# Performance work log

Measured on AMD Instinct MI355X. Metric: run time of the kernel, lower is better.

## Reference

```python
import jax, jax.numpy as jnp
import numpy as np

NEG_SLOPE = 0.2  # PyG GATConv default


def gat_layer(x, src, dst, W, att_src, att_dst, bias, num_nodes):
    """One PyG-style GATConv (concat=True, add_self_loops handled by caller).
    x: [N, F_in], W: [F_in, H*C], att_src/att_dst: [H, C], bias: [H*C].
    """
    H, C = att_src.shape
    h = (x @ W).reshape(num_nodes, H, C)              # [N, H, C]
    a_src = (h * att_src).sum(-1)                     # [N, H]
    a_dst = (h * att_dst).sum(-1)                     # [N, H]
    e = jax.nn.leaky_relu(a_src[src] + a_dst[dst], NEG_SLOPE)  # [E, H]
    # segment softmax over destination neighborhoods
    m = jax.ops.segment_max(e, dst, num_segments=num_nodes)   # [N, H]
    ex = jnp.exp(e - m[dst])
    denom = jax.ops.segment_sum(ex, dst, num_segments=num_nodes)
    alpha = ex / denom[dst]                           # [E, H]
    out = jax.ops.segment_sum(alpha[:, :, None] * h[src], dst,
                              num_segments=num_nodes)  # [N, H, C]
    return out.reshape(num_nodes, H * C) + bias


def setup_inputs() -> dict:
    key = jax.random.key(0)
    ks = jax.random.split(key, 12)
    N, E, D, H = 50000, 800000, 128, 8
    C = D // H
    x = jax.random.normal(ks[0], (N, D), dtype=jnp.float32)
    edge_index = jax.random.randint(ks[1], (2, E), 0, N, dtype=jnp.int64)
    s = 0.1
    return {
        "x": x,
        "edge_index": edge_index,
        "W1": s * jax.random.normal(ks[2], (D, H * C), dtype=jnp.float32),
        "as1": s * jax.random.normal(ks[3], (H, C), dtype=jnp.float32),
        "ad1": s * jax.random.normal(ks[4], (H, C), dtype=jnp.float32),
        "b1": jnp.zeros((H * C,), dtype=jnp.float32),
        "W2": s * jax.random.normal(ks[5], (D, H * C), dtype=jnp.float32),
        "as2": s * jax.random.normal(ks[6], (H, C), dtype=jnp.float32),
        "ad2": s * jax.random.normal(ks[7], (H, C), dtype=jnp.float32),
        "b2": jnp.zeros((H * C,), dtype=jnp.float32),
    }


def reference(x, edge_index, W1, as1, ad1, b1, W2, as2, ad2, b2):
    n = x.shape[0]
    # PyG GATConv default add_self_loops=True
    loop = jnp.arange(n, dtype=edge_index.dtype)
    src = jnp.concatenate([edge_index[0], loop])
    dst = jnp.concatenate([edge_index[1], loop])
    h = jax.nn.relu(gat_layer(x, src, dst, W1, as1, ad1, b1, n))
    # dropout p=0.5 is identity in eval mode
    return gat_layer(h, src, dst, W2, as2, ad2, b2, n)
```

## Files before the change

### kernel.cpp

```cpp
#include <hip/hip_runtime.h>
#include <math.h>

#define D 128
#define H 8
#define C 16
#define NEG_SLOPE 0.2f
#define SCAN_TILE 1024

typedef unsigned short ushortT;
typedef __attribute__((ext_vector_type(8))) short short8;
typedef __attribute__((ext_vector_type(4))) float f32x4;

__device__ __forceinline__ float bf2f(unsigned short v) {
    union { unsigned int i; float f; } c;
    c.i = ((unsigned int)v) << 16;
    return c.f;
}
__device__ __forceinline__ unsigned short f2bf(float f) {
    union { float f; unsigned int i; } c;
    c.f = f;
    unsigned int lsb = (c.i >> 16) & 1u;
    c.i += 0x7fffu + lsb;
    return (unsigned short)(c.i >> 16);
}



__global__ void k_hist(const int* __restrict__ ei, int* cursor,
                       int* __restrict__ rank, int E, int n) {
    int i4 = (blockIdx.x * blockDim.x + threadIdx.x) * 4;
    if (((E & 3) == 0) && i4 + 3 < E) {
        int4 dv = *(const int4*)(ei + (size_t)E + i4);
        int4 r;
        r.x = atomicAdd(cursor + dv.x, 1);
        r.y = atomicAdd(cursor + dv.y, 1);
        r.z = atomicAdd(cursor + dv.z, 1);
        r.w = atomicAdd(cursor + dv.w, 1);
        *(int4*)(rank + i4) = r;
    } else {
        for (int k = i4; k < E && k < i4 + 4; k++)
            rank[k] = atomicAdd(cursor + ei[(size_t)E + k], 1);
    }
}

__device__ __forceinline__ int padc(int c) { return (c + 4) & ~3; }

__global__ __launch_bounds__(256) void k_scan_partial(
    const int* __restrict__ cursor, int* __restrict__ bsum, int n) {
    __shared__ int lds[256];
    int t = threadIdx.x;
    int base = blockIdx.x * SCAN_TILE + t * 4;
    int s = 0;
    if (base + 3 < n) {
        int4 v = *(const int4*)(cursor + base);
        s = padc(v.x) + padc(v.y) + padc(v.z) + padc(v.w);
    } else {
        for (int k = 0; k < 4; k++)
            if (base + k < n) s += padc(cursor[base + k]);
    }
    lds[t] = s;
    __syncthreads();
    for (int st = 128; st > 0; st >>= 1) {
        if (t < st) lds[t] += lds[t + st];
        __syncthreads();
    }
    if (t == 0) bsum[blockIdx.x] = lds[0];
}

__global__ void k_scan_bsum(int* bsum, int nb) {
    if (threadIdx.x == 0 && blockIdx.x == 0) {
        int run = 0;
        for (int i = 0; i < nb; i++) {
            int v = bsum[i];
            bsum[i] = run;
            run += v;
        }
    }
}

__global__ __launch_bounds__(256) void k_scan_final(
    const int* __restrict__ cursor, int* __restrict__ poffs,
    const int* __restrict__ bsum, int* __restrict__ csrsrc, int n) {
    __shared__ int lds[256];
    int t = threadIdx.x;
    int base = blockIdx.x * SCAN_TILE + t * 4;
    int c[4] = {0, 0, 0, 0};
    if (base + 3 < n) {
        int4 q = *(const int4*)(cursor + base);
        c[0] = q.x; c[1] = q.y; c[2] = q.z; c[3] = q.w;
    } else {
        for (int k = 0; k < 4; k++)
            if (base + k < n) c[k] = cursor[base + k];
    }
    int s = padc(c[0]) + padc(c[1]) + padc(c[2]) + padc(c[3]);
    lds[t] = s;
    __syncthreads();
    for (int st = 1; st < 256; st <<= 1) {
        int add = (t >= st) ? lds[t - st] : 0;
        __syncthreads();
        lds[t] += add;
        __syncthreads();
    }
    int run = bsum[blockIdx.x] + ((t == 0) ? 0 : lds[t - 1]);
    if (blockIdx.x == 0 && t == 0) poffs[0] = 0;
#pragma unroll
    for (int k = 0; k < 4; k++) {
        int i = base + k;
        if (i < n) {
            int pv = padc(c[k]);
            csrsrc[run + c[k]] = i;
            for (int k2 = c[k] + 1; k2 < pv; k2++)
                csrsrc[run + k2] = n;
            run += pv;
            poffs[i + 1] = run;
        }
    }
}

__global__ void k_fill(const int* __restrict__ ei, const int* __restrict__ poffs,
                       const int* __restrict__ rank, int* __restrict__ csrsrc,
                       ushortT* __restrict__ hbuf, float* __restrict__ asrc,
                       int E, int n) {
    int tid = blockIdx.x * blockDim.x + threadIdx.x;
    int E4 = (E + 3) >> 2;
    if (tid < E4) {
        int i4 = tid * 4;
        if (((E & 3) == 0) && i4 + 3 < E) {
            int4 sv = *(const int4*)(ei + i4);
            int4 dv = *(const int4*)(ei + (size_t)E + i4);
            int4 rv = *(const int4*)(rank + i4);
            csrsrc[poffs[dv.x] + rv.x] = sv.x;
            csrsrc[poffs[dv.y] + rv.y] = sv.y;
            csrsrc[poffs[dv.z] + rv.z] = sv.z;
            csrsrc[poffs[dv.w] + rv.w] = sv.w;
        } else {
            for (int k = i4; k < E && k < i4 + 4; k++)
                csrsrc[poffs[ei[(size_t)E + k]] + rank[k]] = ei[k];
        }
    } else if (tid == E4) {
        int total = poffs[n];
        for (int k = 0; k < 8; k++) csrsrc[total + k] = n;
        for (int k = 0; k < D; k++) hbuf[(size_t)n * D + k] = 0;
        for (int h = 0; h < H; h++) asrc[n * H + h] = -1e30f;
    }
}


__global__ __launch_bounds__(256) void k_xsplit(
    const float* __restrict__ x, ushortT* __restrict__ xh,
    ushortT* __restrict__ xl, int n, int nt16) {
    int idx = blockIdx.x * 256 + threadIdx.x;
    int r = idx >> 4;
    if (r >= nt16 * 16) return;
    int kb = idx & 15;
    float4 v0 = make_float4(0.f, 0.f, 0.f, 0.f), v1 = v0;
    if (r < n) {
        v0 = ((const float4*)(x + (size_t)r * D + kb * 8))[0];
        v1 = ((const float4*)(x + (size_t)r * D + kb * 8))[1];
    }
    int wt = r >> 4, m = r & 15, kt = kb >> 2, quad = kb & 3;
    int base = ((wt * 4 + kt) * 64 + (m + 16 * quad)) * 8;
    ushort4 h0, l0, h1, l1;
    h0.x = f2bf(v0.x); l0.x = f2bf(v0.x - bf2f(h0.x));
    h0.y = f2bf(v0.y); l0.y = f2bf(v0.y - bf2f(h0.y));
    h0.z = f2bf(v0.z); l0.z = f2bf(v0.z - bf2f(h0.z));
    h0.w = f2bf(v0.w); l0.w = f2bf(v0.w - bf2f(h0.w));
    h1.x = f2bf(v1.x); l1.x = f2bf(v1.x - bf2f(h1.x));
    h1.y = f2bf(v1.y); l1.y = f2bf(v1.y - bf2f(h1.y));
    h1.z = f2bf(v1.z); l1.z = f2bf(v1.z - bf2f(h1.z));
    h1.w = f2bf(v1.w); l1.w = f2bf(v1.w - bf2f(h1.w));
    *(ushort4*)(xh + base) = h0;
    *(ushort4*)(xh + base + 4) = h1;
    *(ushort4*)(xl + base) = l0;
    *(ushort4*)(xl + base + 4) = l1;
}


__global__ __launch_bounds__(256) void k_wprep(
    const float* __restrict__ W1, const float* __restrict__ as1,
    const float* __restrict__ ad1, const float* __restrict__ W2,
    const float* __restrict__ as2, const float* __restrict__ ad2,
    ushortT* __restrict__ wf1_hi, ushortT* __restrict__ wf1_lo,
    ushortT* __restrict__ wf2_hi, ushortT* __restrict__ wf2_lo) {
    int b = blockIdx.x;
    const float *W, *att_s, *att_d;
    ushortT *whi, *wlo;
    int idx;
    if (b < 9) {
        W = W1; att_s = as1; att_d = ad1; whi = wf1_hi; wlo = wf1_lo;
        idx = b * 256 + threadIdx.x;
    } else {
        W = W2; att_s = as2; att_d = ad2; whi = wf2_hi; wlo = wf2_lo;
        idx = (b - 9) * 256 + threadIdx.x;
    }
    if (idx >= 4 * 9 * 64) return;
    int lane = idx & 63;
    int nt = (idx >> 6) % 9;
    int kt = idx / (9 * 64);
    int quad = lane >> 4, ncol = lane & 15;
#pragma unroll
    for (int j = 0; j < 8; j++) {
        int k = kt * 32 + quad * 8 + j;
        float v;
        if (nt < 8) {
            v = W[k * D + nt * 16 + ncol];
        } else {
            const float* att = (ncol < 8) ? att_s : att_d;
            int hd = ncol & 7;
            float s = 0.f;
            for (int c = 0; c < 16; c++)
                s += W[k * D + hd * 16 + c] * att[hd * 16 + c];
            v = s;
        }
        unsigned short hi = f2bf(v);
        unsigned short lo = f2bf(v - bf2f(hi));
        whi[idx * 8 + j] = hi;
        wlo[idx * 8 + j] = lo;
    }
}


__global__ __launch_bounds__(256) void k_gemm_att(
    const ushortT* __restrict__ xh, const ushortT* __restrict__ xl,
    const ushortT* __restrict__ wf_hi, const ushortT* __restrict__ wf_lo,
    ushortT* __restrict__ hout, float* __restrict__ as_,
    float* __restrict__ ad_, int n) {
    int t = threadIdx.x;
    int wt = blockIdx.x * 4 + (t >> 6);
    if (wt * 16 >= n) return;
    int lane = t & 63;

    f32x4 acc[9];
#pragma unroll
    for (int nt = 0; nt < 9; nt++) acc[nt] = (f32x4){0.f, 0.f, 0.f, 0.f};

#pragma unroll
    for (int kt = 0; kt < 4; kt++) {
        const ushortT* ax = xh + (size_t)((wt * 4 + kt) * 64 + lane) * 8;
        short8 a_hi = *(const short8*)ax;
        short8 a_lo = *(const short8*)(xl + (size_t)((wt * 4 + kt) * 64 + lane) * 8);
        const ushortT* bh = wf_hi + (size_t)(kt * 576 + lane) * 8;
        const ushortT* bl = wf_lo + (size_t)(kt * 576 + lane) * 8;
#pragma unroll
        for (int nt = 0; nt < 9; nt++) {
            short8 b_hi = *(const short8*)(bh + nt * 512);
            short8 b_lo = *(const short8*)(bl + nt * 512);
            acc[nt] = __builtin_amdgcn_mfma_f32_16x16x32_bf16(a_hi, b_hi, acc[nt], 0, 0, 0);
            acc[nt] = __builtin_amdgcn_mfma_f32_16x16x32_bf16(a_lo, b_hi, acc[nt], 0, 0, 0);
            acc[nt] = __builtin_amdgcn_mfma_f32_16x16x32_bf16(a_hi, b_lo, acc[nt], 0, 0, 0);
        }
    }

    int q = lane >> 4, ncol = lane & 15;
    int rbase = wt * 16 + q * 4;
#pragma unroll
    for (int nt = 0; nt < 8; nt++) {
#pragma unroll
        for (int reg = 0; reg < 4; reg++) {
            int r = rbase + reg;
            if (r < n) hout[(size_t)r * D + nt * 16 + ncol] = f2bf(acc[nt][reg]);
        }
    }
#pragma unroll
    for (int reg = 0; reg < 4; reg++) {
        int r = rbase + reg;
        if (r < n) {
            float v = acc[8][reg];
            if (ncol < 8) as_[r * H + ncol] = v;
            else          ad_[r * H + (ncol - 8)] = v;
        }
    }
}


__global__ __launch_bounds__(256) void k_aggregate(
    const ushortT* __restrict__ hbuf, const float* __restrict__ asrc,
    const float* __restrict__ adst, const int* __restrict__ csr,
    const int* __restrict__ poffs, const float* __restrict__ bias,
    float* __restrict__ out, ushortT* __restrict__ oh, ushortT* __restrict__ ol,
    int out_mode, int n) {
    int t = threadIdx.x;
    int d = blockIdx.x * 8 + (t >> 5);
    if (d >= n) return;
    int ll = t & 31;
    int h = ll >> 2;

    int off = poffs[d];
    int degp = poffs[d + 1] - off;
    float adh = adst[d * H + h];

    float4 acc0 = make_float4(0.f, 0.f, 0.f, 0.f);
    float4 acc1 = make_float4(0.f, 0.f, 0.f, 0.f);
    float ssum = 0.f;

    int s0 = csr[off + 0], s1 = csr[off + 1], s2 = csr[off + 2], s3 = csr[off + 3];
    for (int j = 0; j < degp; j += 4) {
        int p0 = csr[off + j + 4], p1 = csr[off + j + 5];
        int p2 = csr[off + j + 6], p3 = csr[off + j + 7];
        float e0 = asrc[s0 * H + h] + adh;
        float e1 = asrc[s1 * H + h] + adh;
        float e2 = asrc[s2 * H + h] + adh;
        float e3 = asrc[s3 * H + h] + adh;
        ushort4 u0 = *(const ushort4*)(hbuf + (size_t)s0 * D + ll * 4);
        ushort4 u1 = *(const ushort4*)(hbuf + (size_t)s1 * D + ll * 4);
        ushort4 u2 = *(const ushort4*)(hbuf + (size_t)s2 * D + ll * 4);
        ushort4 u3 = *(const ushort4*)(hbuf + (size_t)s3 * D + ll * 4);
        float w0 = __expf(e0 > 0.f ? e0 : NEG_SLOPE * e0);
        float w1 = __expf(e1 > 0.f ? e1 : NEG_SLOPE * e1);
        float w2 = __expf(e2 > 0.f ? e2 : NEG_SLOPE * e2);
        float w3 = __expf(e3 > 0.f ? e3 : NEG_SLOPE * e3);
        ssum += (w0 + w1) + (w2 + w3);
        acc0.x += w0 * bf2f(u0.x); acc0.y += w0 * bf2f(u0.y);
        acc0.z += w0 * bf2f(u0.z); acc0.w += w0 * bf2f(u0.w);
        acc1.x += w1 * bf2f(u1.x); acc1.y += w1 * bf2f(u1.y);
        acc1.z += w1 * bf2f(u1.z); acc1.w += w1 * bf2f(u1.w);
        acc0.x += w2 * bf2f(u2.x); acc0.y += w2 * bf2f(u2.y);
        acc0.z += w2 * bf2f(u2.z); acc0.w += w2 * bf2f(u2.w);
        acc1.x += w3 * bf2f(u3.x); acc1.y += w3 * bf2f(u3.y);
        acc1.z += w3 * bf2f(u3.z); acc1.w += w3 * bf2f(u3.w);
        s0 = p0; s1 = p1; s2 = p2; s3 = p3;
    }

    float inv = 1.f / ssum;
    float4 b = ((const float4*)bias)[ll];
    float4 r;
    r.x = (acc0.x + acc1.x) * inv + b.x;
    r.y = (acc0.y + acc1.y) * inv + b.y;
    r.z = (acc0.z + acc1.z) * inv + b.z;
    r.w = (acc0.w + acc1.w) * inv + b.w;

    if (out_mode == 0) {
        ((float4*)(out + (size_t)d * D))[ll] = r;
    } else {
        r.x = fmaxf(r.x, 0.f);
        r.y = fmaxf(r.y, 0.f);
        r.z = fmaxf(r.z, 0.f);
        r.w = fmaxf(r.w, 0.f);
        int wt = d >> 4, m = d & 15;
        int kt = ll >> 3, quad = (ll >> 1) & 3, j0 = (ll & 1) * 4;
        int base = ((wt * 4 + kt) * 64 + (m + 16 * quad)) * 8 + j0;
        ushort4 hv, lv;
        hv.x = f2bf(r.x); lv.x = f2bf(r.x - bf2f(hv.x));
        hv.y = f2bf(r.y); lv.y = f2bf(r.y - bf2f(hv.y));
        hv.z = f2bf(r.z); lv.z = f2bf(r.z - bf2f(hv.z));
        hv.w = f2bf(r.w); lv.w = f2bf(r.w - bf2f(hv.w));
        *(ushort4*)(oh + base) = hv;
        *(ushort4*)(ol + base) = lv;
    }
}


extern "C" void kernel_launch(void* const* d_in, const int* in_sizes, int n_in,
                              void* d_out, int out_size, void* d_ws, size_t ws_size,
                              hipStream_t stream) {
    const float* x   = (const float*)d_in[0];
    const int*   ei  = (const int*)d_in[1];
    const float* W1  = (const float*)d_in[2];
    const float* as1 = (const float*)d_in[3];
    const float* ad1 = (const float*)d_in[4];
    const float* b1  = (const float*)d_in[5];
    const float* W2  = (const float*)d_in[6];
    const float* as2 = (const float*)d_in[7];
    const float* ad2 = (const float*)d_in[8];
    const float* b2  = (const float*)d_in[9];
    float* out = (float*)d_out;

    int N = in_sizes[0] / D;
    int E = in_sizes[1] / 2;
    int NT16 = (N + 15) / 16;
    int nb_scan = (N + SCAN_TILE - 1) / SCAN_TILE;
    const int WFN = 4 * 9 * 64 * 8;
    size_t XS = (size_t)NT16 * 2048;

    ushortT* hbuf = (ushortT*)d_ws;
    ushortT* xsh  = hbuf + (size_t)(N + 1) * D;
    ushortT* xsl  = xsh + XS;
    float* asrc = (float*)(xsl + XS);
    float* adst = asrc + (size_t)(N + 1) * H;
    int*   poffs  = (int*)(adst + (size_t)N * H);
    int*   cursor = poffs + ((N + 1 + 3) & ~3);
    int*   bsum   = cursor + ((N + 3) & ~3);
    int*   rank   = bsum + ((nb_scan + 3) & ~3);
    int*   csrsrc = rank + ((E + 3) & ~3);
    ushortT* wf1_hi = (ushortT*)(csrsrc + ((E + 4 * N + 8 + 3) & ~3));
    ushortT* wf1_lo = wf1_hi + WFN;
    ushortT* wf2_hi = wf1_lo + WFN;
    ushortT* wf2_lo = wf2_hi + WFN;

    hipMemsetAsync(cursor, 0, (size_t)N * sizeof(int), stream);

    int nb;
    nb = ((E + 3) / 4 + 255) / 256;
    k_hist<<<nb, 256, 0, stream>>>(ei, cursor, rank, E, N);
    k_scan_partial<<<nb_scan, 256, 0, stream>>>(cursor, bsum, N);
    k_scan_bsum<<<1, 64, 0, stream>>>(bsum, nb_scan);
    k_scan_final<<<nb_scan, 256, 0, stream>>>(cursor, poffs, bsum, csrsrc, N);
    nb = ((E + 3) / 4 + 1 + 255) / 256;
    k_fill<<<nb, 256, 0, stream>>>(ei, poffs, rank, csrsrc, hbuf, asrc, E, N);

    k_wprep<<<18, 256, 0, stream>>>(W1, as1, ad1, W2, as2, ad2,
                                    wf1_hi, wf1_lo, wf2_hi, wf2_lo);
    k_xsplit<<<NT16, 256, 0, stream>>>(x, xsh, xsl, N, NT16);

    int gb = (NT16 + 3) / 4;
    int ab = (N + 7) / 8;
    k_gemm_att<<<gb, 256, 0, stream>>>(xsh, xsl, wf1_hi, wf1_lo, hbuf, asrc, adst, N);
    k_aggregate<<<ab, 256, 0, stream>>>(hbuf, asrc, adst, csrsrc, poffs, b1,
                                        out, xsh, xsl, 1, N);
    k_gemm_att<<<gb, 256, 0, stream>>>(xsh, xsl, wf2_hi, wf2_lo, hbuf, asrc, adst, N);
    k_aggregate<<<ab, 256, 0, stream>>>(hbuf, asrc, adst, csrsrc, poffs, b2,
                                        out, xsh, xsl, 0, N);
}
```

Before: 277.7 us.

## Merge preprocessing kernels and use single-pass decoupled-lookback scan

Merges histogram, weight prep and x split into one launch, and replaces the three-kernel scan with a single kernel that spins on per-block published sums. It also fuses the CSR fill with the first GEMM into one grid of disjoint block ranges. The aim is to cut launch count and serialization gaps between small kernels. The lookback relies on all earlier scan blocks being resident, and sstate is sized to 64 blocks. That fits N=50000 (49 blocks) but would hang or overflow for larger graphs.

```diff
diff --git a/kernel.cpp b/kernel.cpp
--- a/kernel.cpp
+++ b/kernel.cpp
@@ -24,11 +24,14 @@
     return (unsigned short)(c.i >> 16);
 }
 
-
-
-__global__ void k_hist(const int* __restrict__ ei, int* cursor,
-                       int* __restrict__ rank, int E, int n) {
-    int i4 = (blockIdx.x * blockDim.x + threadIdx.x) * 4;
+__device__ __forceinline__ int padc(int c) { return (c + 4) & ~3; }
+
+
+
+__device__ __forceinline__ void hist_part(
+    int tid, const int* __restrict__ ei, int* cursor, int* __restrict__ rank,
+    int E) {
+    int i4 = tid * 4;
     if (((E & 3) == 0) && i4 + 3 < E) {
         int4 dv = *(const int4*)(ei + (size_t)E + i4);
         int4 r;
@@ -43,113 +46,51 @@
     }
 }
 
-__device__ __forceinline__ int padc(int c) { return (c + 4) & ~3; }
-
-__global__ __launch_bounds__(256) void k_scan_partial(
-    const int* __restrict__ cursor, int* __restrict__ bsum, int n) {
-    __shared__ int lds[256];
-    int t = threadIdx.x;
-    int base = blockIdx.x * SCAN_TILE + t * 4;
-    int s = 0;
-    if (base + 3 < n) {
-        int4 v = *(const int4*)(cursor + base);
-        s = padc(v.x) + padc(v.y) + padc(v.z) + padc(v.w);
+__device__ __forceinline__ void wprep_part(
+    int b2, int t, const float* __restrict__ W1, const float* __restrict__ as1,
+    const float* __restrict__ ad1, const float* __restrict__ W2,
+    const float* __restrict__ as2, const float* __restrict__ ad2,
+    ushortT* __restrict__ wf1_hi, ushortT* __restrict__ wf1_lo,
+    ushortT* __restrict__ wf2_hi, ushortT* __restrict__ wf2_lo) {
+    const float *W, *att_s, *att_d;
+    ushortT *whi, *wlo;
+    int idx;
+    if (b2 < 9) {
+        W = W1; att_s = as1; att_d = ad1; whi = wf1_hi; wlo = wf1_lo;
+        idx = b2 * 256 + t;
     } else {
-        for (int k = 0; k < 4; k++)
-            if (base + k < n) s += padc(cursor[base + k]);
-    }
-    lds[t] = s;
-    __syncthreads();
-    for (int st = 128; st > 0; st >>= 1) {
-        if (t < st) lds[t] += lds[t + st];
-        __syncthreads();
-    }
-    if (t == 0) bsum[blockIdx.x] = lds[0];
-}
-
-__global__ void k_scan_bsum(int* bsum, int nb) {
-    if (threadIdx.x == 0 && blockIdx.x == 0) {
-        int run = 0;
-        for (int i = 0; i < nb; i++) {
-            int v = bsum[i];
-            bsum[i] = run;
-            run += v;
-        }
-    }
-}
-
-__global__ __launch_bounds__(256) void k_scan_final(
-    const int* __restrict__ cursor, int* __restrict__ poffs,
-    const int* __restrict__ bsum, int* __restrict__ csrsrc, int n) {
-    __shared__ int lds[256];
-    int t = threadIdx.x;
-    int base = blockIdx.x * SCAN_TILE + t * 4;
-    int c[4] = {0, 0, 0, 0};
-    if (base + 3 < n) {
-        int4 q = *(const int4*)(cursor + base);
-        c[0] = q.x; c[1] = q.y; c[2] = q.z; c[3] = q.w;
-    } else {
-        for (int k = 0; k < 4; k++)
-            if (base + k < n) c[k] = cursor[base + k];
-    }
-    int s = padc(c[0]) + padc(c[1]) + padc(c[2]) + padc(c[3]);
-    lds[t] = s;
-    __syncthreads();
-    for (int st = 1; st < 256; st <<= 1) {
-        int add = (t >= st) ? lds[t - st] : 0;
-        __syncthreads();
-        lds[t] += add;
-        __syncthreads();
-    }
-    int run = bsum[blockIdx.x] + ((t == 0) ? 0 : lds[t - 1]);
-    if (blockIdx.x == 0 && t == 0) poffs[0] = 0;
-#pragma unroll
-    for (int k = 0; k < 4; k++) {
-        int i = base + k;
-        if (i < n) {
-            int pv = padc(c[k]);
-            csrsrc[run + c[k]] = i;
-            for (int k2 = c[k] + 1; k2 < pv; k2++)
-                csrsrc[run + k2] = n;
-            run += pv;
-            poffs[i + 1] = run;
-        }
-    }
-}
-
-__global__ void k_fill(const int* __restrict__ ei, const int* __restrict__ poffs,
-                       const int* __restrict__ rank, int* __restrict__ csrsrc,
-                       ushortT* __restrict__ hbuf, float* __restrict__ asrc,
-                       int E, int n) {
-    int tid = blockIdx.x * blockDim.x + threadIdx.x;
-    int E4 = (E + 3) >> 2;
-    if (tid < E4) {
-        int i4 = tid * 4;
-        if (((E & 3) == 0) && i4 + 3 < E) {
-            int4 sv = *(const int4*)(ei + i4);
-            int4 dv = *(const int4*)(ei + (size_t)E + i4);
-            int4 rv = *(const int4*)(rank + i4);
-            csrsrc[poffs[dv.x] + rv.x] = sv.x;
-            csrsrc[poffs[dv.y] + rv.y] = sv.y;
-            csrsrc[poffs[dv.z] + rv.z] = sv.z;
-            csrsrc[poffs[dv.w] + rv.w] = sv.w;
+        W = W2; att_s = as2; att_d = ad2; whi = wf2_hi; wlo = wf2_lo;
+        idx = (b2 - 9) * 256 + t;
+    }
+    if (idx >= 4 * 9 * 64) return;
+    int lane = idx & 63;
+    int nt = (idx >> 6) % 9;
+    int kt = idx / (9 * 64);
+    int quad = lane >> 4, ncol = lane & 15;
+#pragma unroll
+    for (int j = 0; j < 8; j++) {
+        int k = kt * 32 + quad * 8 + j;
+        float v;
+        if (nt < 8) {
+            v = W[k * D + nt * 16 + ncol];
         } else {
-            for (int k = i4; k < E && k < i4 + 4; k++)
-                csrsrc[poffs[ei[(size_t)E + k]] + rank[k]] = ei[k];
-        }
-    } else if (tid == E4) {
-        int total = poffs[n];
-        for (int k = 0; k < 8; k++) csrsrc[total + k] = n;
-        for (int k = 0; k < D; k++) hbuf[(size_t)n * D + k] = 0;
-        for (int h = 0; h < H; h++) asrc[n * H + h] = -1e30f;
-    }
-}
-
-
-__global__ __launch_bounds__(256) void k_xsplit(
-    const float* __restrict__ x, ushortT* __restrict__ xh,
+            const float* att = (ncol < 8) ? att_s : att_d;
+            int hd = ncol & 7;
+            float s = 0.f;
+            for (int c = 0; c < 16; c++)
+                s += W[k * D + hd * 16 + c] * att[hd * 16 + c];
+            v = s;
+        }
+        unsigned short hi = f2bf(v);
+        unsigned short lo = f2bf(v - bf2f(hi));
+        whi[idx * 8 + j] = hi;
+        wlo[idx * 8 + j] = lo;
+    }
+}
+
+__device__ __forceinline__ void xsplit_part(
+    int idx, const float* __restrict__ x, ushortT* __restrict__ xh,
     ushortT* __restrict__ xl, int n, int nt16) {
-    int idx = blockIdx.x * 256 + threadIdx.x;
     int r = idx >> 4;
     if (r >= nt16 * 16) return;
     int kb = idx & 15;
@@ -175,47 +116,172 @@
     *(ushort4*)(xl + base + 4) = l1;
 }
 
-
-__global__ __launch_bounds__(256) void k_wprep(
+__global__ __launch_bounds__(256) void k_prep(
+    const int* __restrict__ ei, int* cursor, int* __restrict__ rank, int E,
+    const float* __restrict__ x, ushortT* __restrict__ xh,
+    ushortT* __restrict__ xl, int n, int nt16,
     const float* __restrict__ W1, const float* __restrict__ as1,
     const float* __restrict__ ad1, const float* __restrict__ W2,
     const float* __restrict__ as2, const float* __restrict__ ad2,
     ushortT* __restrict__ wf1_hi, ushortT* __restrict__ wf1_lo,
-    ushortT* __restrict__ wf2_hi, ushortT* __restrict__ wf2_lo) {
+    ushortT* __restrict__ wf2_hi, ushortT* __restrict__ wf2_lo, int nbh) {
     int b = blockIdx.x;
-    const float *W, *att_s, *att_d;
-    ushortT *whi, *wlo;
-    int idx;
-    if (b < 9) {
-        W = W1; att_s = as1; att_d = ad1; whi = wf1_hi; wlo = wf1_lo;
-        idx = b * 256 + threadIdx.x;
+    int t = threadIdx.x;
+    if (b < nbh) {
+        hist_part(b * 256 + t, ei, cursor, rank, E);
+    } else if (b < nbh + 18) {
+        wprep_part(b - nbh, t, W1, as1, ad1, W2, as2, ad2,
+                   wf1_hi, wf1_lo, wf2_hi, wf2_lo);
     } else {
-        W = W2; att_s = as2; att_d = ad2; whi = wf2_hi; wlo = wf2_lo;
-        idx = (b - 9) * 256 + threadIdx.x;
-    }
-    if (idx >= 4 * 9 * 64) return;
-    int lane = idx & 63;
-    int nt = (idx >> 6) % 9;
-    int kt = idx / (9 * 64);
-    int quad = lane >> 4, ncol = lane & 15;
-#pragma unroll
-    for (int j = 0; j < 8; j++) {
-        int k = kt * 32 + quad * 8 + j;
-        float v;
-        if (nt < 8) {
-            v = W[k * D + nt * 16 + ncol];
+        xsplit_part((b - nbh - 18) * 256 + t, x, xh, xl, n, nt16);
+    }
+}
+
+
+__global__ __launch_bounds__(256) void k_scan_lb(
+    const int* __restrict__ cursor, int* __restrict__ poffs,
+    int* __restrict__ sstate, int* __restrict__ csrsrc, int n) {
+    __shared__ int lds[256];
+    __shared__ int bprefix;
+    int t = threadIdx.x;
+    int b = blockIdx.x;
+    int base = b * SCAN_TILE + t * 4;
+    int c[4] = {0, 0, 0, 0};
+    if (base + 3 < n) {
+        int4 q = *(const int4*)(cursor + base);
+        c[0] = q.x; c[1] = q.y; c[2] = q.z; c[3] = q.w;
+    } else {
+        for (int k = 0; k < 4; k++)
+            if (base + k < n) c[k] = cursor[base + k];
+    }
+    int s = padc(c[0]) + padc(c[1]) + padc(c[2]) + padc(c[3]);
+    lds[t] = s;
+    __syncthreads();
+    for (int st = 1; st < 256; st <<= 1) {
+        int add = (t >= st) ? lds[t - st] : 0;
+        __syncthreads();
+        lds[t] += add;
+        __syncthreads();
+    }
+    if (t == 0)
+        __hip_atomic_store(&sstate[b], lds[255] | (1 << 30),
+                           __ATOMIC_RELEASE, __HIP_MEMORY_SCOPE_AGENT);
+    if (t < 64) {
+        int v = 0;
+        if (t < b) {
+            int x;
+            do {
+                x = __hip_atomic_load(&sstate[t], __ATOMIC_RELAXED,
+                                      __HIP_MEMORY_SCOPE_AGENT);
+            } while (!(x & (1 << 30)));
+            v = x & 0x3FFFFFFF;
+        }
+#pragma unroll
+        for (int o = 32; o > 0; o >>= 1) v += __shfl_down(v, o);
+        if (t == 0) bprefix = v;
+    }
+    __syncthreads();
+    int run = bprefix + ((t == 0) ? 0 : lds[t - 1]);
+    if (b == 0 && t == 0) poffs[0] = 0;
+#pragma unroll
+    for (int k = 0; k < 4; k++) {
+        int i = base + k;
+        if (i < n) {
+            int pv = padc(c[k]);
+            csrsrc[run + c[k]] = i;
+            for (int k2 = c[k] + 1; k2 < pv; k2++)
+                csrsrc[run + k2] = n;
+            run += pv;
+            poffs[i + 1] = run;
+        }
+    }
+}
+
+
+__device__ __forceinline__ void gemm_wave(
+    int wt, int lane, const ushortT* __restrict__ xh,
+    const ushortT* __restrict__ xl, const ushortT* __restrict__ wf_hi,
+    const ushortT* __restrict__ wf_lo, ushortT* __restrict__ hout,
+    float* __restrict__ as_, float* __restrict__ ad_, int n) {
+    f32x4 acc[9];
+#pragma unroll
+    for (int nt = 0; nt < 9; nt++) acc[nt] = (f32x4){0.f, 0.f, 0.f, 0.f};
+
+#pragma unroll
+    for (int kt = 0; kt < 4; kt++) {
+        short8 a_hi = *(const short8*)(xh + (size_t)((wt * 4 + kt) * 64 + lane) * 8);
+        short8 a_lo = *(const short8*)(xl + (size_t)((wt * 4 + kt) * 64 + lane) * 8);
+        const ushortT* bh = wf_hi + (size_t)(kt * 576 + lane) * 8;
+        const ushortT* bl = wf_lo + (size_t)(kt * 576 + lane) * 8;
+#pragma unroll
+        for (int nt = 0; nt < 9; nt++) {
+            short8 b_hi = *(const short8*)(bh + nt * 512);
+            short8 b_lo = *(const short8*)(bl + nt * 512);
+            acc[nt] = __builtin_amdgcn_mfma_f32_16x16x32_bf16(a_hi, b_hi, acc[nt], 0, 0, 0);
+            acc[nt] = __builtin_amdgcn_mfma_f32_16x16x32_bf16(a_lo, b_hi, acc[nt], 0, 0, 0);
+            acc[nt] = __builtin_amdgcn_mfma_f32_16x16x32_bf16(a_hi, b_lo, acc[nt], 0, 0, 0);
+        }
+    }
+
+    int q = lane >> 4, ncol = lane & 15;
+    int rbase = wt * 16 + q * 4;
+#pragma unroll
+    for (int nt = 0; nt < 8; nt++) {
+#pragma unroll
+        for (int reg = 0; reg < 4; reg++) {
+            int r = rbase + reg;
+            if (r < n) hout[(size_t)r * D + nt * 16 + ncol] = f2bf(acc[nt][reg]);
+        }
+    }
+#pragma unroll
+    for (int reg = 0; reg < 4; reg++) {
+        int r = rbase + reg;
+        if (r < n) {
+            float v = acc[8][reg];
+            if (ncol < 8) as_[r * H + ncol] = v;
+            else          ad_[r * H + (ncol - 8)] = v;
+        }
+    }
+}
+
+
+__global__ __launch_bounds__(256) void k_fillgemm(
+    const int* __restrict__ ei, const int* __restrict__ poffs,
+    const int* __restrict__ rank, int* __restrict__ csrsrc,
+    ushortT* __restrict__ hbuf_s, float* __restrict__ asrc_s, int E,
+    const ushortT* __restrict__ xh, const ushortT* __restrict__ xl,
+    const ushortT* __restrict__ wf_hi, const ushortT* __restrict__ wf_lo,
+    ushortT* __restrict__ hout, float* __restrict__ as_,
+    float* __restrict__ ad_, int n, int gb) {
+    int b = blockIdx.x;
+    int t = threadIdx.x;
+    if (b < gb) {
+        int wt = b * 4 + (t >> 6);
+        if (wt * 16 < n)
+            gemm_wave(wt, t & 63, xh, xl, wf_hi, wf_lo, hout, as_, ad_, n);
+        return;
+    }
+    int tid = (b - gb) * 256 + t;
+    int E4 = (E + 3) >> 2;
+    if (tid < E4) {
+        int i4 = tid * 4;
+        if (((E & 3) == 0) && i4 + 3 < E) {
+            int4 sv = *(const int4*)(ei + i4);
+            int4 dv = *(const int4*)(ei + (size_t)E + i4);
+            int4 rv = *(const int4*)(rank + i4);
+            csrsrc[poffs[dv.x] + rv.x] = sv.x;
+            csrsrc[poffs[dv.y] + rv.y] = sv.y;
+            csrsrc[poffs[dv.z] + rv.z] = sv.z;
+            csrsrc[poffs[dv.w] + rv.w] = sv.w;
         } else {
-            const float* att = (ncol < 8) ? att_s : att_d;
-            int hd = ncol & 7;
-            float s = 0.f;
-            for (int c = 0; c < 16; c++)
-                s += W[k * D + hd * 16 + c] * att[hd * 16 + c];
-            v = s;
-        }
-        unsigned short hi = f2bf(v);
-        unsigned short lo = f2bf(v - bf2f(hi));
-        whi[idx * 8 + j] = hi;
-        wlo[idx * 8 + j] = lo;
+            for (int k = i4; k < E && k < i4 + 4; k++)
+                csrsrc[poffs[ei[(size_t)E + k]] + rank[k]] = ei[k];
+        }
+    } else if (tid == E4) {
+        int total = poffs[n];
+        for (int k = 0; k < 8; k++) csrsrc[total + k] = n;
+        for (int k = 0; k < D; k++) hbuf_s[(size_t)n * D + k] = 0;
+        for (int h = 0; h < H; h++) asrc_s[n * H + h] = -1e30f;
     }
 }
 
@@ -228,48 +294,7 @@
     int t = threadIdx.x;
     int wt = blockIdx.x * 4 + (t >> 6);
     if (wt * 16 >= n) return;
-    int lane = t & 63;
-
-    f32x4 acc[9];
-#pragma unroll
-    for (int nt = 0; nt < 9; nt++) acc[nt] = (f32x4){0.f, 0.f, 0.f, 0.f};
-
-#pragma unroll
-    for (int kt = 0; kt < 4; kt++) {
-        const ushortT* ax = xh + (size_t)((wt * 4 + kt) * 64 + lane) * 8;
-        short8 a_hi = *(const short8*)ax;
-        short8 a_lo = *(const short8*)(xl + (size_t)((wt * 4 + kt) * 64 + lane) * 8);
-        const ushortT* bh = wf_hi + (size_t)(kt * 576 + lane) * 8;
-        const ushortT* bl = wf_lo + (size_t)(kt * 576 + lane) * 8;
-#pragma unroll
-        for (int nt = 0; nt < 9; nt++) {
-            short8 b_hi = *(const short8*)(bh + nt * 512);
-            short8 b_lo = *(const short8*)(bl + nt * 512);
-            acc[nt] = __builtin_amdgcn_mfma_f32_16x16x32_bf16(a_hi, b_hi, acc[nt], 0, 0, 0);
-            acc[nt] = __builtin_amdgcn_mfma_f32_16x16x32_bf16(a_lo, b_hi, acc[nt], 0, 0, 0);
-            acc[nt] = __builtin_amdgcn_mfma_f32_16x16x32_bf16(a_hi, b_lo, acc[nt], 0, 0, 0);
-        }
-    }
-
-    int q = lane >> 4, ncol = lane & 15;
-    int rbase = wt * 16 + q * 4;
-#pragma unroll
-    for (int nt = 0; nt < 8; nt++) {
-#pragma unroll
-        for (int reg = 0; reg < 4; reg++) {
-            int r = rbase + reg;
-            if (r < n) hout[(size_t)r * D + nt * 16 + ncol] = f2bf(acc[nt][reg]);
-        }
-    }
-#pragma unroll
-    for (int reg = 0; reg < 4; reg++) {
-        int r = rbase + reg;
-        if (r < n) {
-            float v = acc[8][reg];
-            if (ncol < 8) as_[r * H + ncol] = v;
-            else          ad_[r * H + (ncol - 8)] = v;
-        }
-    }
+    gemm_wave(wt, t & 63, xh, xl, wf_hi, wf_lo, hout, as_, ad_, n);
 }
 
 
@@ -371,6 +396,7 @@
     int nb_scan = (N + SCAN_TILE - 1) / SCAN_TILE;
     const int WFN = 4 * 9 * 64 * 8;
     size_t XS = (size_t)NT16 * 2048;
+    int E4 = (E + 3) >> 2;
 
     ushortT* hbuf = (ushortT*)d_ws;
     ushortT* xsh  = hbuf + (size_t)(N + 1) * D;
@@ -379,32 +405,30 @@
     float* adst = asrc + (size_t)(N + 1) * H;
     int*   poffs  = (int*)(adst + (size_t)N * H);
     int*   cursor = poffs + ((N + 1 + 3) & ~3);
-    int*   bsum   = cursor + ((N + 3) & ~3);
-    int*   rank   = bsum + ((nb_scan + 3) & ~3);
+    int*   sstate = cursor + ((N + 3) & ~3);
+    int*   rank   = sstate + 64;
     int*   csrsrc = rank + ((E + 3) & ~3);
     ushortT* wf1_hi = (ushortT*)(csrsrc + ((E + 4 * N + 8 + 3) & ~3));
     ushortT* wf1_lo = wf1_hi + WFN;
     ushortT* wf2_hi = wf1_lo + WFN;
     ushortT* wf2_lo = wf2_hi + WFN;
 
-    hipMemsetAsync(cursor, 0, (size_t)N * sizeof(int), stream);
-
-    int nb;
-    nb = ((E + 3) / 4 + 255) / 256;
-    k_hist<<<nb, 256, 0, stream>>>(ei, cursor, rank, E, N);
-    k_scan_partial<<<nb_scan, 256, 0, stream>>>(cursor, bsum, N);
-    k_scan_bsum<<<1, 64, 0, stream>>>(bsum, nb_scan);
-    k_scan_final<<<nb_scan, 256, 0, stream>>>(cursor, poffs, bsum, csrsrc, N);
-    nb = ((E + 3) / 4 + 1 + 255) / 256;
-    k_fill<<<nb, 256, 0, stream>>>(ei, poffs, rank, csrsrc, hbuf, asrc, E, N);
-
-    k_wprep<<<18, 256, 0, stream>>>(W1, as1, ad1, W2, as2, ad2,
-                                    wf1_hi, wf1_lo, wf2_hi, wf2_lo);
-    k_xsplit<<<NT16, 256, 0, stream>>>(x, xsh, xsl, N, NT16);
+    hipMemsetAsync(cursor, 0, (size_t)(((N + 3) & ~3) + 64) * sizeof(int), stream);
+
+    int nbh = (E4 + 255) / 256;
+    int nbx = (NT16 * 16 * 16 + 255) / 256;
+    k_prep<<<nbh + 18 + nbx, 256, 0, stream>>>(
+        ei, cursor, rank, E, x, xsh, xsl, N, NT16,
+        W1, as1, ad1, W2, as2, ad2, wf1_hi, wf1_lo, wf2_hi, wf2_lo, nbh);
+
+    k_scan_lb<<<nb_scan, 256, 0, stream>>>(cursor, poffs, sstate, csrsrc, N);
 
     int gb = (NT16 + 3) / 4;
+    int nf = (E4 + 1 + 255) / 256;
     int ab = (N + 7) / 8;
-    k_gemm_att<<<gb, 256, 0, stream>>>(xsh, xsl, wf1_hi, wf1_lo, hbuf, asrc, adst, N);
+    k_fillgemm<<<gb + nf, 256, 0, stream>>>(
+        ei, poffs, rank, csrsrc, hbuf, asrc, E,
+        xsh, xsl, wf1_hi, wf1_lo, hbuf, asrc, adst, N, gb);
     k_aggregate<<<ab, 256, 0, stream>>>(hbuf, asrc, adst, csrsrc, poffs, b1,
                                         out, xsh, xsl, 1, N);
     k_gemm_att<<<gb, 256, 0, stream>>>(xsh, xsl, wf2_hi, wf2_lo, hbuf, asrc, adst, N);
```

Result: faster. 255.0 us (-8.2%).
